# Kernel tuning notes

Hardware: AMD Instinct MI355X
Metric: run time of the kernel (lower is better)

The kernel has to match this reference:

```python
import jax, jax.numpy as jnp
import numpy as np

B, C_IN, N_NODES = 128, 64, 1024
N_TRIPLES = 3 * (N_NODES - 1)  # node 0 is the shared zero vector


def _btc(x, idx, w, b):
    # x: [B, C, N]; idx: [B, 3M]; w: [O, C, 3]; b: [O]
    Bv, C, _ = x.shape
    T = idx.shape[1]
    g = jnp.take_along_axis(x, jnp.broadcast_to(idx[:, None, :], (Bv, C, T)), axis=2)
    g = g.reshape(Bv, C, T // 3, 3)  # stride-3 kernel-3 conv == per-triple contraction
    out = jnp.einsum('bcnk,ock->bon', g, w) + b[None, :, None]
    zero = jnp.zeros((Bv, out.shape[1], 1), dtype=out.dtype)
    return jnp.concatenate([zero, out], axis=2)  # re-prepend zero node -> [B, O, N]


def _tln(x):
    mean = jnp.mean(x, axis=(1, 2), keepdims=True)
    std = jnp.std(x, axis=(1, 2), ddof=1, keepdims=True)  # torch.std is unbiased
    return (x - mean) / (std + 1e-5)


def _tower(x, idx, p):
    x = jax.nn.leaky_relu(_tln(_btc(x, idx, p['w_conv1'], p['b_conv1'])), 0.01)
    x = jax.nn.leaky_relu(_tln(_btc(x, idx, p['w_conv2'], p['b_conv2'])), 0.01)
    x = _tln(_btc(x, idx, p['w_conv3'], p['b_conv3']))
    x = jnp.max(x, axis=2)  # DynamicPooling -> [B, 64]
    x = jax.nn.leaky_relu(x @ p['w_fc1'].T + p['b_fc1'], 0.01)
    return x @ p['w_fc2'].T + p['b_fc2']  # [B, 1]  (Dropout is identity at eval)


def setup_inputs() -> dict:
    key = jax.random.key(0)
    ks = jax.random.split(key, 12)
    s = 0.05
    return {
        'data1': jax.random.normal(ks[0], (B, C_IN, N_NODES), jnp.float32),
        'idx1': jax.random.randint(ks[1], (B, N_TRIPLES, 1), 0, N_NODES, dtype=jnp.int64)
                if jax.config.jax_enable_x64 else
                jax.random.randint(ks[1], (B, N_TRIPLES, 1), 0, N_NODES).astype(jnp.int32),
        'data2': jax.random.normal(ks[2], (B, C_IN, N_NODES), jnp.float32),
        'idx2': jax.random.randint(ks[3], (B, N_TRIPLES, 1), 0, N_NODES).astype(jnp.int32),
        'w_conv1': jax.random.normal(ks[4], (256, C_IN, 3), jnp.float32) * s,
        'b_conv1': jnp.zeros((256,), jnp.float32),
        'w_conv2': jax.random.normal(ks[5], (128, 256, 3), jnp.float32) * s,
        'b_conv2': jnp.zeros((128,), jnp.float32),
        'w_conv3': jax.random.normal(ks[6], (64, 128, 3), jnp.float32) * s,
        'b_conv3': jnp.zeros((64,), jnp.float32),
        'w_fc1': jax.random.normal(ks[7], (32, 64), jnp.float32) * s,
        'b_fc1': jnp.zeros((32,), jnp.float32),
        'w_fc2': jax.random.normal(ks[8], (1, 32), jnp.float32) * s,
        'b_fc2': jnp.zeros((1,), jnp.float32),
    }


def reference(data1, idx1, data2, idx2,
              w_conv1, b_conv1, w_conv2, b_conv2, w_conv3, b_conv3,
              w_fc1, b_fc1, w_fc2, b_fc2):
    p = dict(w_conv1=w_conv1, b_conv1=b_conv1, w_conv2=w_conv2, b_conv2=b_conv2,
             w_conv3=w_conv3, b_conv3=b_conv3, w_fc1=w_fc1, b_fc1=b_fc1,
             w_fc2=w_fc2, b_fc2=b_fc2)
    y1 = _tower(data1, idx1[..., 0], p)
    y2 = _tower(data2, idx2[..., 0], p)
    return jnp.squeeze(jax.nn.sigmoid(y1 - y2), axis=1)  # [B]
```

## Files before the change

kernel.cpp:

```cpp
#include <hip/hip_runtime.h>
#include <math.h>

typedef __attribute__((ext_vector_type(8))) short short8;
typedef __attribute__((ext_vector_type(4))) float f32x4;
typedef __attribute__((ext_vector_type(2))) float f32x2;

#define LRELU(x) ((x) > 0.0f ? (x) : 0.01f * (x))

__device__ __forceinline__ float bf2f(unsigned short h) {
    return __uint_as_float(((unsigned int)h) << 16);
}
__device__ __forceinline__ unsigned short f2bf(float f) {
    unsigned int u = __float_as_uint(f);
    return (unsigned short)((u + 0x7FFFu + ((u >> 16) & 1u)) >> 16);
}
__device__ __forceinline__ unsigned int pack_bf16_pair(float lo, float hi) {
    unsigned int ul = __float_as_uint(lo) + 0x8000u;
    unsigned int uh = __float_as_uint(hi) + 0x8000u;
    return (ul >> 16) | (uh & 0xFFFF0000u);
}
__device__ __forceinline__ float2 stats_from(const float* sums, int b, float count) {
    float s = sums[2 * b], q = sums[2 * b + 1];
    float mean = s / count;
    float var = (q - s * s / count) / (count - 1.0f);
    var = fmaxf(var, 0.0f);
    return make_float2(mean, 1.0f / (sqrtf(var) + 1e-5f));
}
__device__ __forceinline__ void atomicMaxF(float* a, float v) {
    if (v >= 0.0f) atomicMax((int*)a, __float_as_int(v));
    else           atomicMin((unsigned int*)a, __float_as_uint(v));
}
__device__ __forceinline__ unsigned int norm_pair(unsigned int u, float a, float c) {
    f32x2 v;
    v.x = __uint_as_float(u << 16);
    v.y = __uint_as_float(u & 0xFFFF0000u);
    v = v * a + c;
    f32x2 m = v * 0.01f;
    v = __builtin_elementwise_max(v, m);
    return pack_bf16_pair(v.x, v.y);
}
__device__ __forceinline__ uint4 norm8(uint4 v, float a, float c) {
    v.x = norm_pair(v.x, a, c); v.y = norm_pair(v.y, a, c);
    v.z = norm_pair(v.z, a, c); v.w = norm_pair(v.w, a, c);
    return v;
}
__device__ __forceinline__ uint2 fp8x4_nl(unsigned int u, float a, float c) {
    f32x2 lo = __builtin_amdgcn_cvt_pk_f32_fp8(u, false);
    f32x2 hi = __builtin_amdgcn_cvt_pk_f32_fp8(u, true);
    lo = lo * a + c; hi = hi * a + c;
    f32x2 ml = lo * 0.01f, mh = hi * 0.01f;
    lo = __builtin_elementwise_max(lo, ml);
    hi = __builtin_elementwise_max(hi, mh);
    uint2 r;
    r.x = pack_bf16_pair(lo.x, lo.y);
    r.y = pack_bf16_pair(hi.x, hi.y);
    return r;
}

template <int MT, int WM>
__device__ __forceinline__ void mfma_step(const unsigned short* wt, const unsigned short* gt,
                                          f32x4 (&acc)[MT][4],
                                          int wo, int wn, int quad, int l15, int blkid)
{
#pragma unroll
    for (int st = 0; st < 2; ++st) {
        short8 af[MT], bfv[4];
        const int qb = st * 4 + quad;
#pragma unroll
        for (int i = 0; i < MT; i++) {
            const int orow = wo * WM + i * 16 + l15;
            af[i] = *(const short8*)&wt[orow * 64 + ((qb ^ blkid) << 3)];
        }
#pragma unroll
        for (int t = 0; t < 4; t++) {
            const int nrow = wn * 64 + t * 16 + l15;
            bfv[t] = *(const short8*)&gt[nrow * 64 + ((qb ^ blkid) << 3)];
        }
#pragma unroll
        for (int i = 0; i < MT; i++)
#pragma unroll
            for (int t = 0; t < 4; t++)
                acc[i][t] = __builtin_amdgcn_mfma_f32_16x16x32_bf16(
                    af[i], bfv[t], acc[i][t], 0, 0, 0);
    }
}

__global__ void prep_weights(const float* __restrict__ w, unsigned short* __restrict__ wq,
                             int O, int Cin)
{
    const int K = 3 * Cin, total = O * K;
    for (int i = blockIdx.x * blockDim.x + threadIdx.x; i < total;
         i += gridDim.x * blockDim.x) {
        int o = i / K, kp = i - o * K;
        int j = kp / Cin, c = kp - j * Cin;
        wq[i] = f2bf(w[(o * Cin + c) * 3 + j]);
    }
}

__global__ __launch_bounds__(256) void transpose_in(const float* __restrict__ inA,
                                                    const float* __restrict__ inB,
                                                    unsigned short* __restrict__ xT)
{
    const int b = blockIdx.y, n0 = blockIdx.x * 64;
    const float* in = (b >= 128 ? inB : inA) + ((size_t)(b & 127) * 64) * 1024;
    const int tid = threadIdx.x;
    __shared__ float tile[64][65];
    const int nn = tid & 63, cw = tid >> 6;
#pragma unroll
    for (int i = 0; i < 16; i++) {
        int c = i * 4 + cw;
        tile[c][nn] = in[(size_t)c * 1024 + n0 + nn];
    }
    __syncthreads();
    const int n = tid >> 2, cp = (tid & 3) * 16;
    unsigned int pk[8];
#pragma unroll
    for (int i = 0; i < 8; i++) {
        unsigned short lo = f2bf(tile[cp + 2 * i][n]);
        unsigned short hi = f2bf(tile[cp + 2 * i + 1][n]);
        pk[i] = (unsigned int)lo | ((unsigned int)hi << 16);
    }
    unsigned short* dst = xT + ((size_t)b * 1024 + n0 + n) * 64 + cp;
    uint4 v0 = {pk[0], pk[1], pk[2], pk[3]};
    uint4 v1 = {pk[4], pk[5], pk[6], pk[7]};
    *(uint4*)dst = v0;
    *(uint4*)(dst + 8) = v1;
}

template <int BM, bool POOL, bool NORM, bool FP8IN, bool FP8OUT>
__global__ __launch_bounds__(256, 2) void conv_mfma(
    const void* __restrict__ xTv,
    const int* __restrict__ idxA,
    const int* __restrict__ idxB,
    const unsigned short* __restrict__ wq,
    const float* __restrict__ bias,
    void* __restrict__ out,
    float* __restrict__ sums,
    float* __restrict__ pmax,
    const float* __restrict__ normSums,
    float normCount, int Cin, int cinShift, int O, int K)
{
    constexpr int WM = BM / 2, MT = WM / 16;
    constexpr int NW = (BM == 128) ? 4 : 2;
    const int b   = blockIdx.x;
    const int o0  = blockIdx.y * BM;
    const int nt0 = blockIdx.z << 7;
    const int tid = threadIdx.x;
    const int lane = tid & 63, wave = tid >> 6;
    const int wo = wave & 1, wn = wave >> 1;
    const int quad = lane >> 4, l15 = lane & 15;
    const int blkid = lane & 7;

    __shared__ __align__(16) unsigned short wt[BM * 64];
    __shared__ __align__(16) unsigned short gt[128 * 64];

    f32x4 acc[MT][4];
#pragma unroll
    for (int i = 0; i < MT; i++)
#pragma unroll
        for (int t = 0; t < 4; t++) acc[i][t] = (f32x4){0.f, 0.f, 0.f, 0.f};

    const unsigned short* xTb16 = (const unsigned short*)xTv + (((size_t)b) << 10) * (size_t)Cin;
    const unsigned char*  xTb8  = (const unsigned char*)xTv  + (((size_t)b) << 10) * (size_t)Cin;
    const int* idxb = (b >= 128 ? idxB : idxA) + (size_t)(b & 127) * 3069;

    float na = 1.0f, nc = 0.0f;
    if (NORM) {
        float2 st = stats_from(normSums, b, normCount);
        na = st.y; nc = -st.x * st.y;
    }

    const int gr = tid >> 1, gh = tid & 1;
    int s0, s1, s2;
    {
        int n = nt0 + gr;
        int t0 = (n == 0) ? 0 : (n - 1);
        s0 = idxb[3 * t0]; s1 = idxb[3 * t0 + 1]; s2 = idxb[3 * t0 + 2];
    }
    const int wr   = (BM == 128) ? (tid >> 1) : (tid >> 2);
    const int wseg = (BM == 128) ? (tid & 1) : (tid & 3);
    const unsigned short* wrow = wq + (size_t)(o0 + wr) * K + wseg * (NW * 8);
    const int gswz = gr & 7, wswz = wr & 7;

    uint4 g0A, g1A, g2A, g3A, w0A, w1A, w2A, w3A;
    uint4 g0B, g1B, g2B, g3B, w0B, w1B, w2B, w3B;

#define LOADC(S, KC) {                                                           \
        const int k64_ = (KC) << 6;                                              \
        const int j_   = k64_ >> cinShift;                                       \
        const int c0_  = k64_ & (Cin - 1);                                       \
        const int src_ = (j_ == 0) ? s0 : ((j_ == 1) ? s1 : s2);                 \
        if (FP8IN) {                                                             \
            const uint4* gp_ = (const uint4*)(xTb8 + (size_t)src_ * Cin + c0_ + gh * 32); \
            g0##S = gp_[0]; g1##S = gp_[1];                                      \
        } else {                                                                 \
            const uint4* gp_ = (const uint4*)(xTb16 + (size_t)src_ * Cin + c0_ + gh * 32); \
            g0##S = gp_[0]; g1##S = gp_[1]; g2##S = gp_[2]; g3##S = gp_[3];      \
        }                                                                        \
        const uint4* wp_ = (const uint4*)(wrow + k64_);                          \
        w0##S = wp_[0]; w1##S = wp_[1];                                          \
        if (NW == 4) { w2##S = wp_[2]; w3##S = wp_[3]; }                         \
    }

#define STAGE(S) {                                                               \
        uint4 h0, h1, h2, h3;                                                    \
        if (FP8IN) {                                                             \
            uint2 p0 = fp8x4_nl(g0##S.x, na, nc), p1 = fp8x4_nl(g0##S.y, na, nc);\
            uint2 p2 = fp8x4_nl(g0##S.z, na, nc), p3 = fp8x4_nl(g0##S.w, na, nc);\
            h0.x = p0.x; h0.y = p0.y; h0.z = p1.x; h0.w = p1.y;                  \
            h1.x = p2.x; h1.y = p2.y; h1.z = p3.x; h1.w = p3.y;                  \
            p0 = fp8x4_nl(g1##S.x, na, nc); p1 = fp8x4_nl(g1##S.y, na, nc);      \
            p2 = fp8x4_nl(g1##S.z, na, nc); p3 = fp8x4_nl(g1##S.w, na, nc);      \
            h2.x = p0.x; h2.y = p0.y; h2.z = p1.x; h2.w = p1.y;                  \
            h3.x = p2.x; h3.y = p2.y; h3.z = p3.x; h3.w = p3.y;                  \
        } else {                                                                 \
            h0 = g0##S; h1 = g1##S; h2 = g2##S; h3 = g3##S;                      \
            if (NORM) {                                                          \
                h0 = norm8(h0, na, nc); h1 = norm8(h1, na, nc);                  \
                h2 = norm8(h2, na, nc); h3 = norm8(h3, na, nc);                  \
            }                                                                    \
        }                                                                        \
        *(uint4*)&gt[gr * 64 + (((gh << 2) | 0) ^ gswz) * 8] = h0;               \
        *(uint4*)&gt[gr * 64 + (((gh << 2) | 1) ^ gswz) * 8] = h1;               \
        *(uint4*)&gt[gr * 64 + (((gh << 2) | 2) ^ gswz) * 8] = h2;               \
        *(uint4*)&gt[gr * 64 + (((gh << 2) | 3) ^ gswz) * 8] = h3;               \
        *(uint4*)&wt[wr * 64 + ((wseg * NW + 0) ^ wswz) * 8] = w0##S;            \
        *(uint4*)&wt[wr * 64 + ((wseg * NW + 1) ^ wswz) * 8] = w1##S;            \
        if (NW == 4) {                                                           \
            *(uint4*)&wt[wr * 64 + ((wseg * NW + 2) ^ wswz) * 8] = w2##S;        \
            *(uint4*)&wt[wr * 64 + ((wseg * NW + 3) ^ wswz) * 8] = w3##S;        \
        }                                                                        \
    }

    const int nChunks = K >> 6;
    LOADC(A, 0);
    if (nChunks > 1) LOADC(B, 1);
    int kc = 0;
    for (; kc + 2 <= nChunks; kc += 2) {
        if (kc) __syncthreads();
        STAGE(A);
        if (kc + 2 < nChunks) LOADC(A, kc + 2);
        __syncthreads();
        mfma_step<MT, WM>(wt, gt, acc, wo, wn, quad, l15, blkid);
        __syncthreads();
        STAGE(B);
        if (kc + 3 < nChunks) LOADC(B, kc + 3);
        __syncthreads();
        mfma_step<MT, WM>(wt, gt, acc, wo, wn, quad, l15, blkid);
    }
    if (kc < nChunks) {
        __syncthreads();
        STAGE(A);
        __syncthreads();
        mfma_step<MT, WM>(wt, gt, acc, wo, wn, quad, l15, blkid);
    }
#undef LOADC
#undef STAGE

    float lsum = 0.f, lsq = 0.f;
#pragma unroll
    for (int i = 0; i < MT; i++) {
        const int ob = o0 + wo * WM + i * 16 + quad * 4;
        const float4 bv = *(const float4*)(bias + ob);
        float mx0 = -1e30f, mx1 = -1e30f, mx2 = -1e30f, mx3 = -1e30f;
#pragma unroll
        for (int t = 0; t < 4; t++) {
            const int n = nt0 + wn * 64 + t * 16 + l15;
            float v0 = acc[i][t][0] + bv.x;
            float v1 = acc[i][t][1] + bv.y;
            float v2 = acc[i][t][2] + bv.z;
            float v3 = acc[i][t][3] + bv.w;
            if (n == 0) { v0 = v1 = v2 = v3 = 0.f; }
            lsum += v0 + v1 + v2 + v3;
            lsq  += v0 * v0 + v1 * v1 + v2 * v2 + v3 * v3;
            if (POOL) {
                mx0 = fmaxf(mx0, v0); mx1 = fmaxf(mx1, v1);
                mx2 = fmaxf(mx2, v2); mx3 = fmaxf(mx3, v3);
            } else if (FP8OUT) {
                int r = __builtin_amdgcn_cvt_pk_fp8_f32(v0, v1, 0, false);
                r = __builtin_amdgcn_cvt_pk_fp8_f32(v2, v3, r, true);
                *(unsigned int*)&((unsigned char*)out)[((size_t)b * 1024 + n) * O + ob] =
                    (unsigned int)r;
            } else {
                uint2 pk;
                pk.x = pack_bf16_pair(v0, v1);
                pk.y = pack_bf16_pair(v2, v3);
                *(uint2*)&((unsigned short*)out)[((size_t)b * 1024 + n) * O + ob] = pk;
            }
        }
        if (POOL) {
#pragma unroll
            for (int off = 1; off < 16; off <<= 1) {
                mx0 = fmaxf(mx0, __shfl_xor(mx0, off));
                mx1 = fmaxf(mx1, __shfl_xor(mx1, off));
                mx2 = fmaxf(mx2, __shfl_xor(mx2, off));
                mx3 = fmaxf(mx3, __shfl_xor(mx3, off));
            }
            if (l15 == 0) {
                atomicMaxF(&pmax[(size_t)b * 64 + ob + 0], mx0);
                atomicMaxF(&pmax[(size_t)b * 64 + ob + 1], mx1);
                atomicMaxF(&pmax[(size_t)b * 64 + ob + 2], mx2);
                atomicMaxF(&pmax[(size_t)b * 64 + ob + 3], mx3);
            }
        }
    }
#pragma unroll
    for (int off = 32; off > 0; off >>= 1) {
        lsum += __shfl_down(lsum, off);
        lsq  += __shfl_down(lsq, off);
    }
    float* red = (float*)wt;
    if (lane == 0) { red[wave] = lsum; red[4 + wave] = lsq; }
    __syncthreads();
    if (tid == 0) {
        atomicAdd(&sums[2 * b + 0], red[0] + red[1] + red[2] + red[3]);
        atomicAdd(&sums[2 * b + 1], red[4] + red[5] + red[6] + red[7]);
    }
}

__global__ __launch_bounds__(64) void fc_head(
    const float* __restrict__ pmax, const float* __restrict__ sums3, float count,
    const float* __restrict__ w_fc1, const float* __restrict__ b_fc1,
    const float* __restrict__ w_fc2, const float* __restrict__ b_fc2,
    float* __restrict__ y)
{
    const int b = blockIdx.x, t = threadIdx.x;
    __shared__ float pooled[64];
    __shared__ float hid[32];
    float2 s = stats_from(sums3, b, count);
    pooled[t] = (pmax[(size_t)b * 64 + t] - s.x) * s.y;
    __syncthreads();
    if (t < 32) {
        float h = b_fc1[t];
#pragma unroll
        for (int c = 0; c < 64; c++) h += pooled[c] * w_fc1[t * 64 + c];
        hid[t] = LRELU(h);
    }
    __syncthreads();
    if (t == 0) {
        float v = b_fc2[0];
#pragma unroll
        for (int c = 0; c < 32; c++) v += hid[c] * w_fc2[c];
        y[b] = v;
    }
}

__global__ void sigmoid_diff(const float* __restrict__ y1,
                             const float* __restrict__ y2,
                             float* __restrict__ out)
{
    int b = threadIdx.x;
    if (b < 128) out[b] = 1.0f / (1.0f + expf(-(y1[b] - y2[b])));
}

extern "C" void kernel_launch(void* const* d_in, const int* in_sizes, int n_in,
                              void* d_out, int out_size, void* d_ws, size_t ws_size,
                              hipStream_t stream)
{
    const float* data1 = (const float*)d_in[0];
    const int*   idx1  = (const int*)d_in[1];
    const float* data2 = (const float*)d_in[2];
    const int*   idx2  = (const int*)d_in[3];
    const float* w1 = (const float*)d_in[4];
    const float* b1 = (const float*)d_in[5];
    const float* w2 = (const float*)d_in[6];
    const float* b2 = (const float*)d_in[7];
    const float* w3 = (const float*)d_in[8];
    const float* b3 = (const float*)d_in[9];
    const float* wfc1 = (const float*)d_in[10];
    const float* bfc1 = (const float*)d_in[11];
    const float* wfc2 = (const float*)d_in[12];
    const float* bfc2 = (const float*)d_in[13];

    const size_t needM = (size_t)256 * 1024 * (64 * 2 + 256 * 1 + 128 * 2) + 768 * 1024;
    const bool merged = ws_size >= needM;
    const int nB = merged ? 256 : 128;
    const size_t szXT = (size_t)nB * 1024 * 64 * 2;
    const size_t szA1 = (size_t)nB * 1024 * 256;
    const size_t szA2 = (size_t)nB * 1024 * 128 * 2;

    char* ws = (char*)d_ws;
    unsigned short* xT = (unsigned short*)ws;
    unsigned char*  a1 = (unsigned char*)(ws + szXT);
    unsigned short* a2 = (unsigned short*)(ws + szXT + szA1);
    char* tail = ws + szXT + szA1 + szA2;
    unsigned short* wq1 = (unsigned short*)tail;
    unsigned short* wq2 = (unsigned short*)(tail + 128 * 1024);
    unsigned short* wq3 = (unsigned short*)(tail + 384 * 1024);
    float* sums = (float*)(tail + 448 * 1024);
    float* pmax = (float*)(tail + 512 * 1024);
    float* yv   = (float*)(tail + 640 * 1024);

    prep_weights<<<96, 256, 0, stream>>>(w1, wq1, 256, 64);
    prep_weights<<<96, 256, 0, stream>>>(w2, wq2, 128, 256);
    prep_weights<<<96, 256, 0, stream>>>(w3, wq3, 64, 128);

    const int nIter = merged ? 1 : 2;
    for (int t = 0; t < nIter; ++t) {
        const float* dA = (merged || t == 0) ? data1 : data2;
        const float* dB = merged ? data2 : dA;
        const int* iA = (merged || t == 0) ? idx1 : idx2;
        const int* iB = merged ? idx2 : iA;
        float* s1 = sums;
        float* s2 = sums + nB * 2;
        float* s3 = sums + nB * 4;

        hipMemsetAsync(sums, 0, 3 * (size_t)nB * 2 * sizeof(float), stream);
        hipMemsetAsync(pmax, 0xFF, (size_t)nB * 64 * sizeof(float), stream);

        transpose_in<<<dim3(16, nB), 256, 0, stream>>>(dA, dB, xT);

        conv_mfma<128, false, false, false, true><<<dim3(nB, 2, 8), 256, 0, stream>>>(
            xT, iA, iB, wq1, b1, a1, s1, nullptr, nullptr, 0.0f, 64, 6, 256, 192);

        conv_mfma<128, false, true, true, false><<<dim3(nB, 1, 8), 256, 0, stream>>>(
            a1, iA, iB, wq2, b2, a2, s2, nullptr, s1, 256.0f * 1024.0f, 256, 8, 128, 768);

        conv_mfma<64, true, true, false, false><<<dim3(nB, 1, 8), 256, 0, stream>>>(
            a2, iA, iB, wq3, b3, nullptr, s3, pmax, s2, 128.0f * 1024.0f, 128, 7, 64, 384);

        fc_head<<<nB, 64, 0, stream>>>(pmax, s3, 64.0f * 1024.0f,
                                       wfc1, bfc1, wfc2, bfc2,
                                       yv + (merged ? 0 : t * 128));
    }
    sigmoid_diff<<<1, 128, 0, stream>>>(yv, yv + 128, (float*)d_out);
}
```

Baseline: 325.4 us.

## Run conv2 as FP8 MFMA with separate in-place norm+activation pass

Layer-1 activations, already stored as FP8, are now normalized and leaky-ReLU'd in place by a new elementwise kernel and re-quantized to FP8. Conv2 weights are also quantized to FP8, and a dedicated conv2 kernel uses fp8×fp8 MFMA with 128-byte K chunks, halving LDS and global bytes per K step and removing the per-gather FP8-to-bf16 conversion. The cost is an extra full read/write pass over a1, plus extra precision loss from quantizing both weights and normalized activations to FP8.

```diff
diff --git a/kernel.cpp b/kernel.cpp
--- a/kernel.cpp
+++ b/kernel.cpp
@@ -44,17 +44,16 @@
     v.z = norm_pair(v.z, a, c); v.w = norm_pair(v.w, a, c);
     return v;
 }
-__device__ __forceinline__ uint2 fp8x4_nl(unsigned int u, float a, float c) {
+__device__ __forceinline__ unsigned int fp8x4_nact(unsigned int u, float a, float c) {
     f32x2 lo = __builtin_amdgcn_cvt_pk_f32_fp8(u, false);
     f32x2 hi = __builtin_amdgcn_cvt_pk_f32_fp8(u, true);
     lo = lo * a + c; hi = hi * a + c;
     f32x2 ml = lo * 0.01f, mh = hi * 0.01f;
     lo = __builtin_elementwise_max(lo, ml);
     hi = __builtin_elementwise_max(hi, mh);
-    uint2 r;
-    r.x = pack_bf16_pair(lo.x, lo.y);
-    r.y = pack_bf16_pair(hi.x, hi.y);
-    return r;
+    int r = __builtin_amdgcn_cvt_pk_fp8_f32(lo.x, lo.y, 0, false);
+    r = __builtin_amdgcn_cvt_pk_fp8_f32(hi.x, hi.y, r, true);
+    return (unsigned int)r;
 }
 
 template <int MT, int WM>
@@ -97,6 +96,33 @@
     }
 }
 
+__global__ void prep_weights_fp8(const float* __restrict__ w, unsigned char* __restrict__ wq,
+                                 int O, int Cin)
+{
+    const int K = 3 * Cin, total = (O * K) >> 2;
+    for (int i = blockIdx.x * blockDim.x + threadIdx.x; i < total;
+         i += gridDim.x * blockDim.x) {
+        const int e0 = i << 2;
+        const int o = e0 / K, kp0 = e0 - o * K;
+        float f0, f1, f2, f3;
+        {
+            int kp = kp0 + 0, j = kp / Cin, c = kp - j * Cin; f0 = w[(o * Cin + c) * 3 + j];
+        }
+        {
+            int kp = kp0 + 1, j = kp / Cin, c = kp - j * Cin; f1 = w[(o * Cin + c) * 3 + j];
+        }
+        {
+            int kp = kp0 + 2, j = kp / Cin, c = kp - j * Cin; f2 = w[(o * Cin + c) * 3 + j];
+        }
+        {
+            int kp = kp0 + 3, j = kp / Cin, c = kp - j * Cin; f3 = w[(o * Cin + c) * 3 + j];
+        }
+        int r = __builtin_amdgcn_cvt_pk_fp8_f32(f0, f1, 0, false);
+        r = __builtin_amdgcn_cvt_pk_fp8_f32(f2, f3, r, true);
+        *(unsigned int*)&wq[e0] = (unsigned int)r;
+    }
+}
+
 __global__ __launch_bounds__(256) void transpose_in(const float* __restrict__ inA,
                                                     const float* __restrict__ inB,
                                                     unsigned short* __restrict__ xT)
@@ -125,6 +151,27 @@
     uint4 v1 = {pk[4], pk[5], pk[6], pk[7]};
     *(uint4*)dst = v0;
     *(uint4*)(dst + 8) = v1;
+}
+
+__global__ __launch_bounds__(256) void norm_act_fp8(unsigned char* __restrict__ a,
+                                                    const float* __restrict__ sums,
+                                                    float count)
+{
+    const int b = blockIdx.y;
+    float2 st = stats_from(sums, b, count);
+    const float na = st.y, nc = -st.x * st.y;
+    uint4* p = (uint4*)(a + ((size_t)b << 18));
+    const int base = blockIdx.x * 256 + threadIdx.x;
+#pragma unroll
+    for (int it = 0; it < 4; ++it) {
+        const int idx = base + it * 4096;
+        uint4 v = p[idx];
+        v.x = fp8x4_nact(v.x, na, nc);
+        v.y = fp8x4_nact(v.y, na, nc);
+        v.z = fp8x4_nact(v.z, na, nc);
+        v.w = fp8x4_nact(v.w, na, nc);
+        p[idx] = v;
+    }
 }
 
 template <int BM, bool POOL, bool NORM, bool FP8IN, bool FP8OUT>
@@ -204,21 +251,10 @@
 
 #define STAGE(S) {                                                               \
         uint4 h0, h1, h2, h3;                                                    \
-        if (FP8IN) {                                                             \
-            uint2 p0 = fp8x4_nl(g0##S.x, na, nc), p1 = fp8x4_nl(g0##S.y, na, nc);\
-            uint2 p2 = fp8x4_nl(g0##S.z, na, nc), p3 = fp8x4_nl(g0##S.w, na, nc);\
-            h0.x = p0.x; h0.y = p0.y; h0.z = p1.x; h0.w = p1.y;                  \
-            h1.x = p2.x; h1.y = p2.y; h1.z = p3.x; h1.w = p3.y;                  \
-            p0 = fp8x4_nl(g1##S.x, na, nc); p1 = fp8x4_nl(g1##S.y, na, nc);      \
-            p2 = fp8x4_nl(g1##S.z, na, nc); p3 = fp8x4_nl(g1##S.w, na, nc);      \
-            h2.x = p0.x; h2.y = p0.y; h2.z = p1.x; h2.w = p1.y;                  \
-            h3.x = p2.x; h3.y = p2.y; h3.z = p3.x; h3.w = p3.y;                  \
-        } else {                                                                 \
-            h0 = g0##S; h1 = g1##S; h2 = g2##S; h3 = g3##S;                      \
-            if (NORM) {                                                          \
-                h0 = norm8(h0, na, nc); h1 = norm8(h1, na, nc);                  \
-                h2 = norm8(h2, na, nc); h3 = norm8(h3, na, nc);                  \
-            }                                                                    \
+        h0 = g0##S; h1 = g1##S; h2 = g2##S; h3 = g3##S;                          \
+        if (NORM) {                                                              \
+            h0 = norm8(h0, na, nc); h1 = norm8(h1, na, nc);                      \
+            h2 = norm8(h2, na, nc); h3 = norm8(h3, na, nc);                      \
         }                                                                        \
         *(uint4*)&gt[gr * 64 + (((gh << 2) | 0) ^ gswz) * 8] = h0;               \
         *(uint4*)&gt[gr * 64 + (((gh << 2) | 1) ^ gswz) * 8] = h1;               \
@@ -318,6 +354,166 @@
     }
 }
 
+__global__ __launch_bounds__(256, 2) void conv2_fp8(
+    const unsigned char* __restrict__ a1,
+    const int* __restrict__ idxA,
+    const int* __restrict__ idxB,
+    const unsigned char* __restrict__ wq8,
+    const float* __restrict__ bias,
+    unsigned short* __restrict__ out,
+    float* __restrict__ sums)
+{
+    const int b   = blockIdx.x;
+    const int nt0 = blockIdx.z << 7;
+    const int tid = threadIdx.x;
+    const int lane = tid & 63, wave = tid >> 6;
+    const int wo = wave & 1, wn = wave >> 1;
+    const int quad = lane >> 4, l15 = lane & 15;
+    const int blkid = lane & 7;
+
+    __shared__ __align__(16) unsigned char wt8[128 * 128];
+    __shared__ __align__(16) unsigned char gt8[128 * 128];
+
+    f32x4 acc[4][4];
+#pragma unroll
+    for (int i = 0; i < 4; i++)
+#pragma unroll
+        for (int t = 0; t < 4; t++) acc[i][t] = (f32x4){0.f, 0.f, 0.f, 0.f};
+
+    const unsigned char* xb = a1 + (((size_t)b) << 10) * 256;
+    const int* idxb = (b >= 128 ? idxB : idxA) + (size_t)(b & 127) * 3069;
+
+    const int gr = tid >> 1, gh = tid & 1;
+    int si0, si1, si2;
+    {
+        int n = nt0 + gr;
+        int t0 = (n == 0) ? 0 : (n - 1);
+        si0 = idxb[3 * t0]; si1 = idxb[3 * t0 + 1]; si2 = idxb[3 * t0 + 2];
+    }
+    const unsigned char* wrow = wq8 + (size_t)gr * 768 + gh * 64;
+    const int swz = gr & 7;
+
+    uint4 g0A, g1A, g2A, g3A, w0A, w1A, w2A, w3A;
+    uint4 g0B, g1B, g2B, g3B, w0B, w1B, w2B, w3B;
+
+#define LOADC2(S, KC) {                                                          \
+        const int j_  = (KC) >> 1;                                               \
+        const int c0_ = ((KC) & 1) << 7;                                         \
+        const int src_ = (j_ == 0) ? si0 : ((j_ == 1) ? si1 : si2);              \
+        const uint4* gp_ = (const uint4*)(xb + (size_t)src_ * 256 + c0_ + gh * 64); \
+        g0##S = gp_[0]; g1##S = gp_[1]; g2##S = gp_[2]; g3##S = gp_[3];          \
+        const uint4* wp_ = (const uint4*)(wrow + (KC) * 128);                    \
+        w0##S = wp_[0]; w1##S = wp_[1]; w2##S = wp_[2]; w3##S = wp_[3];          \
+    }
+
+#define STAGE2(S) {                                                              \
+        *(uint4*)&gt8[gr * 128 + (((gh << 2) | 0) ^ swz) * 16] = g0##S;          \
+        *(uint4*)&gt8[gr * 128 + (((gh << 2) | 1) ^ swz) * 16] = g1##S;          \
+        *(uint4*)&gt8[gr * 128 + (((gh << 2) | 2) ^ swz) * 16] = g2##S;          \
+        *(uint4*)&gt8[gr * 128 + (((gh << 2) | 3) ^ swz) * 16] = g3##S;          \
+        *(uint4*)&wt8[gr * 128 + (((gh << 2) | 0) ^ swz) * 16] = w0##S;          \
+        *(uint4*)&wt8[gr * 128 + (((gh << 2) | 1) ^ swz) * 16] = w1##S;          \
+        *(uint4*)&wt8[gr * 128 + (((gh << 2) | 2) ^ swz) * 16] = w2##S;          \
+        *(uint4*)&wt8[gr * 128 + (((gh << 2) | 3) ^ swz) * 16] = w3##S;          \
+    }
+
+#define MFMA_STEP2 {                                                             \
+        _Pragma("unroll")                                                        \
+        for (int st = 0; st < 4; ++st) {                                         \
+            long af0, af1, af2, af3, bf0, bf1, bf2, bf3;                         \
+            const int qb = st * 4 + quad;                                        \
+            const int cg = qb >> 1, ch = (qb & 1) << 3;                          \
+            {                                                                    \
+                const int r0 = wo * 64 + 0 * 16 + l15;                           \
+                af0 = *(const long*)&wt8[r0 * 128 + ((cg ^ blkid) << 4) + ch];   \
+                const int r1 = wo * 64 + 1 * 16 + l15;                           \
+                af1 = *(const long*)&wt8[r1 * 128 + ((cg ^ blkid) << 4) + ch];   \
+                const int r2 = wo * 64 + 2 * 16 + l15;                           \
+                af2 = *(const long*)&wt8[r2 * 128 + ((cg ^ blkid) << 4) + ch];   \
+                const int r3 = wo * 64 + 3 * 16 + l15;                           \
+                af3 = *(const long*)&wt8[r3 * 128 + ((cg ^ blkid) << 4) + ch];   \
+                const int n0 = wn * 64 + 0 * 16 + l15;                           \
+                bf0 = *(const long*)&gt8[n0 * 128 + ((cg ^ blkid) << 4) + ch];   \
+                const int n1 = wn * 64 + 1 * 16 + l15;                           \
+                bf1 = *(const long*)&gt8[n1 * 128 + ((cg ^ blkid) << 4) + ch];   \
+                const int n2 = wn * 64 + 2 * 16 + l15;                           \
+                bf2 = *(const long*)&gt8[n2 * 128 + ((cg ^ blkid) << 4) + ch];   \
+                const int n3 = wn * 64 + 3 * 16 + l15;                           \
+                bf3 = *(const long*)&gt8[n3 * 128 + ((cg ^ blkid) << 4) + ch];   \
+            }                                                                    \
+            acc[0][0] = __builtin_amdgcn_mfma_f32_16x16x32_fp8_fp8(af0, bf0, acc[0][0], 0, 0, 0); \
+            acc[0][1] = __builtin_amdgcn_mfma_f32_16x16x32_fp8_fp8(af0, bf1, acc[0][1], 0, 0, 0); \
+            acc[0][2] = __builtin_amdgcn_mfma_f32_16x16x32_fp8_fp8(af0, bf2, acc[0][2], 0, 0, 0); \
+            acc[0][3] = __builtin_amdgcn_mfma_f32_16x16x32_fp8_fp8(af0, bf3, acc[0][3], 0, 0, 0); \
+            acc[1][0] = __builtin_amdgcn_mfma_f32_16x16x32_fp8_fp8(af1, bf0, acc[1][0], 0, 0, 0); \
+            acc[1][1] = __builtin_amdgcn_mfma_f32_16x16x32_fp8_fp8(af1, bf1, acc[1][1], 0, 0, 0); \
+            acc[1][2] = __builtin_amdgcn_mfma_f32_16x16x32_fp8_fp8(af1, bf2, acc[1][2], 0, 0, 0); \
+            acc[1][3] = __builtin_amdgcn_mfma_f32_16x16x32_fp8_fp8(af1, bf3, acc[1][3], 0, 0, 0); \
+            acc[2][0] = __builtin_amdgcn_mfma_f32_16x16x32_fp8_fp8(af2, bf0, acc[2][0], 0, 0, 0); \
+            acc[2][1] = __builtin_amdgcn_mfma_f32_16x16x32_fp8_fp8(af2, bf1, acc[2][1], 0, 0, 0); \
+            acc[2][2] = __builtin_amdgcn_mfma_f32_16x16x32_fp8_fp8(af2, bf2, acc[2][2], 0, 0, 0); \
+            acc[2][3] = __builtin_amdgcn_mfma_f32_16x16x32_fp8_fp8(af2, bf3, acc[2][3], 0, 0, 0); \
+            acc[3][0] = __builtin_amdgcn_mfma_f32_16x16x32_fp8_fp8(af3, bf0, acc[3][0], 0, 0, 0); \
+            acc[3][1] = __builtin_amdgcn_mfma_f32_16x16x32_fp8_fp8(af3, bf1, acc[3][1], 0, 0, 0); \
+            acc[3][2] = __builtin_amdgcn_mfma_f32_16x16x32_fp8_fp8(af3, bf2, acc[3][2], 0, 0, 0); \
+            acc[3][3] = __builtin_amdgcn_mfma_f32_16x16x32_fp8_fp8(af3, bf3, acc[3][3], 0, 0, 0); \
+        }                                                                        \
+    }
+
+    LOADC2(A, 0);
+    LOADC2(B, 1);
+    int kc = 0;
+    for (; kc + 2 <= 6; kc += 2) {
+        if (kc) __syncthreads();
+        STAGE2(A);
+        if (kc + 2 < 6) LOADC2(A, kc + 2);
+        __syncthreads();
+        MFMA_STEP2;
+        __syncthreads();
+        STAGE2(B);
+        if (kc + 3 < 6) LOADC2(B, kc + 3);
+        __syncthreads();
+        MFMA_STEP2;
+    }
+#undef LOADC2
+#undef STAGE2
+#undef MFMA_STEP2
+
+    float lsum = 0.f, lsq = 0.f;
+#pragma unroll
+    for (int i = 0; i < 4; i++) {
+        const int ob = wo * 64 + i * 16 + quad * 4;
+        const float4 bv = *(const float4*)(bias + ob);
+#pragma unroll
+        for (int t = 0; t < 4; t++) {
+            const int n = nt0 + wn * 64 + t * 16 + l15;
+            float v0 = acc[i][t][0] + bv.x;
+            float v1 = acc[i][t][1] + bv.y;
+            float v2 = acc[i][t][2] + bv.z;
+            float v3 = acc[i][t][3] + bv.w;
+            if (n == 0) { v0 = v1 = v2 = v3 = 0.f; }
+            lsum += v0 + v1 + v2 + v3;
+            lsq  += v0 * v0 + v1 * v1 + v2 * v2 + v3 * v3;
+            uint2 pk;
+            pk.x = pack_bf16_pair(v0, v1);
+            pk.y = pack_bf16_pair(v2, v3);
+            *(uint2*)&out[((size_t)b * 1024 + n) * 128 + ob] = pk;
+        }
+    }
+#pragma unroll
+    for (int off = 32; off > 0; off >>= 1) {
+        lsum += __shfl_down(lsum, off);
+        lsq  += __shfl_down(lsq, off);
+    }
+    float* red = (float*)wt8;
+    if (lane == 0) { red[wave] = lsum; red[4 + wave] = lsq; }
+    __syncthreads();
+    if (tid == 0) {
+        atomicAdd(&sums[2 * b + 0], red[0] + red[1] + red[2] + red[3]);
+        atomicAdd(&sums[2 * b + 1], red[4] + red[5] + red[6] + red[7]);
+    }
+}
+
 __global__ __launch_bounds__(64) void fc_head(
     const float* __restrict__ pmax, const float* __restrict__ sums3, float count,
     const float* __restrict__ w_fc1, const float* __restrict__ b_fc1,
@@ -385,14 +581,14 @@
     unsigned short* a2 = (unsigned short*)(ws + szXT + szA1);
     char* tail = ws + szXT + szA1 + szA2;
     unsigned short* wq1 = (unsigned short*)tail;
-    unsigned short* wq2 = (unsigned short*)(tail + 128 * 1024);
+    unsigned char*  wq2f8 = (unsigned char*)(tail + 128 * 1024);
     unsigned short* wq3 = (unsigned short*)(tail + 384 * 1024);
     float* sums = (float*)(tail + 448 * 1024);
     float* pmax = (float*)(tail + 512 * 1024);
     float* yv   = (float*)(tail + 640 * 1024);
 
     prep_weights<<<96, 256, 0, stream>>>(w1, wq1, 256, 64);
-    prep_weights<<<96, 256, 0, stream>>>(w2, wq2, 128, 256);
+    prep_weights_fp8<<<96, 256, 0, stream>>>(w2, wq2f8, 128, 256);
     prep_weights<<<96, 256, 0, stream>>>(w3, wq3, 64, 128);
 
     const int nIter = merged ? 1 : 2;
@@ -413,8 +609,10 @@
         conv_mfma<128, false, false, false, true><<<dim3(nB, 2, 8), 256, 0, stream>>>(
             xT, iA, iB, wq1, b1, a1, s1, nullptr, nullptr, 0.0f, 64, 6, 256, 192);
 
-        conv_mfma<128, false, true, true, false><<<dim3(nB, 1, 8), 256, 0, stream>>>(
-            a1, iA, iB, wq2, b2, a2, s2, nullptr, s1, 256.0f * 1024.0f, 256, 8, 128, 768);
+        norm_act_fp8<<<dim3(16, nB), 256, 0, stream>>>(a1, s1, 256.0f * 1024.0f);
+
+        conv2_fp8<<<dim3(nB, 1, 8), 256, 0, stream>>>(
+            a1, iA, iB, wq2f8, b2, a2, s2);
 
         conv_mfma<64, true, true, false, false><<<dim3(nB, 1, 8), 256, 0, stream>>>(
             a2, iA, iB, wq3, b3, nullptr, s3, pmax, s2, 128.0f * 1024.0f, 128, 7, 64, 384);
```

After: 324.1 us. About the same (-0.4%).
